# Kernel tuning notes

Hardware: AMD Instinct MI355X
Metric: run time of the kernel (lower is better)

Reference implementation:

```python
import jax, jax.numpy as jnp
import numpy as np

ACT_BIT = 8
W_BIT = 8
EPS = 1e-8


def ste_round(x):
    # straight-through round (matches torch STE quant autograd)
    return x + jax.lax.stop_gradient(jnp.round(x) - x)


def quant_act(x):
    """Per-tensor symmetric 8-bit activation quantization (HAWQ QuantAct)."""
    n = 2 ** (ACT_BIT - 1) - 1  # 127
    x_max = jax.lax.stop_gradient(jnp.max(jnp.abs(x)))
    scale = jnp.maximum(x_max, EPS) / n
    x_int = jnp.clip(ste_round(x / scale), -n - 1, n)
    return x_int * scale, scale


def quant_linear(x_q, act_scale, weight, bias):
    """Per-channel symmetric 8-bit weight quant + integer matmul + fused dequant."""
    n = 2 ** (W_BIT - 1) - 1  # 127
    w_max = jax.lax.stop_gradient(jnp.max(jnp.abs(weight), axis=1, keepdims=True))  # [out,1]
    w_scale = jnp.maximum(w_max, EPS) / n                                            # [out,1]
    w_int = jnp.clip(ste_round(weight / w_scale), -n - 1, n)                         # [out,in]
    bias_scale = w_scale[:, 0] * act_scale                                           # [out]
    b_int = ste_round(bias / bias_scale)                                             # [out]
    x_int = x_q / act_scale                                   # integer-valued float, [..., in]
    out_int = jnp.einsum('...i,oi->...o', x_int, w_int)       # int8-domain GEMM in float
    return (out_int + b_int) * bias_scale                     # fused dequant


def setup_inputs() -> dict:
    key = jax.random.key(0)
    k1, k2, k3 = jax.random.split(key, 3)
    L, B, Q, D, O = 6, 8, 1024, 1024, 1024
    hs = jax.random.normal(k1, (L, B, Q, D), dtype=jnp.float32)
    weight = jax.random.normal(k2, (O, D), dtype=jnp.float32) * 0.02
    bias = jax.random.normal(k3, (O,), dtype=jnp.float32) * 0.02
    return {"hs": hs, "weight": weight, "bias": bias}


def reference(hs, weight, bias):
    x_q, act_scale = quant_act(hs)
    return quant_linear(x_q, act_scale, weight, bias)
```

## Files before the change

kernel.cpp:

```cpp
#include <hip/hip_runtime.h>
#include <stdint.h>

typedef int i32x4 __attribute__((ext_vector_type(4)));

#define K_DIM 1024
#define BM 256
#define BN 256
#define BKK 64
#define NKT (K_DIM / BKK)


__device__ __forceinline__ int quant1(float v, float inv) {
  float t = rintf(v * inv);
  t = fminf(fmaxf(t, -128.0f), 127.0f);
  return (int)t;
}

__device__ __forceinline__ void gld_lds16(const signed char* g, signed char* l) {
  typedef const __attribute__((address_space(1))) unsigned int* gp_t;
  typedef __attribute__((address_space(3))) unsigned int* lp_t;
  __builtin_amdgcn_global_load_lds((gp_t)(const void*)g, (lp_t)(void*)l, 16, 0, 0);
}

#define SB __builtin_amdgcn_sched_barrier(0)
#define BAR __builtin_amdgcn_s_barrier()
#define WAIT_LGKM0 asm volatile("s_waitcnt lgkmcnt(0)" ::: "memory")

__global__ void absmax_part(const float* __restrict__ x, float* __restrict__ parts,
                            long long n4) {
  long long i = (long long)blockIdx.x * blockDim.x + threadIdx.x;
  const long long stride = (long long)gridDim.x * blockDim.x;
  const float4* x4 = (const float4*)x;
  float m = 0.0f;
  for (; i < n4; i += stride) {
    float4 v = x4[i];
    m = fmaxf(m, fmaxf(fmaxf(fabsf(v.x), fabsf(v.y)), fmaxf(fabsf(v.z), fabsf(v.w))));
  }
#pragma unroll
  for (int off = 32; off > 0; off >>= 1) m = fmaxf(m, __shfl_down(m, off, 64));
  __shared__ float sm[4];
  const int lane = threadIdx.x & 63, wid = threadIdx.x >> 6;
  if (lane == 0) sm[wid] = m;
  __syncthreads();
  if (threadIdx.x == 0)
    parts[blockIdx.x] = fmaxf(fmaxf(sm[0], sm[1]), fmaxf(sm[2], sm[3]));
}

__global__ void absmax_fin(const float* __restrict__ parts, unsigned int* __restrict__ amax_u,
                           int nparts) {
  const int t = threadIdx.x;
  float m = 0.0f;
  for (int i = t; i < nparts; i += 256) m = fmaxf(m, parts[i]);
#pragma unroll
  for (int off = 32; off > 0; off >>= 1) m = fmaxf(m, __shfl_down(m, off, 64));
  __shared__ float sm[4];
  const int lane = t & 63, wid = t >> 6;
  if (lane == 0) sm[wid] = m;
  __syncthreads();
  if (t == 0)
    amax_u[0] = __float_as_uint(fmaxf(fmaxf(sm[0], sm[1]), fmaxf(sm[2], sm[3])));
}

__global__ void wquant_kernel(const float* __restrict__ w, const float* __restrict__ bias,
                              const unsigned int* __restrict__ amax_u,
                              signed char* __restrict__ wq,
                              float* __restrict__ bscale, float* __restrict__ bint) {
  const int o = blockIdx.x;
  const int t = threadIdx.x;
  float4 v = ((const float4*)(w + (size_t)o * K_DIM))[t];
  float m = fmaxf(fmaxf(fabsf(v.x), fabsf(v.y)), fmaxf(fabsf(v.z), fabsf(v.w)));
#pragma unroll
  for (int off = 32; off > 0; off >>= 1) m = fmaxf(m, __shfl_down(m, off, 64));
  __shared__ float sm[4];
  __shared__ float s_scale;
  const int lane = t & 63, wid = t >> 6;
  if (lane == 0) sm[wid] = m;
  __syncthreads();
  if (t == 0) {
    float wm = fmaxf(fmaxf(sm[0], sm[1]), fmaxf(sm[2], sm[3]));
    float wsc = fmaxf(wm, 1e-8f) / 127.0f;
    float asc = fmaxf(__uint_as_float(*amax_u), 1e-8f) / 127.0f;
    float bsc = wsc * asc;
    bscale[o] = bsc;
    bint[o] = rintf(bias[o] / bsc);
    s_scale = wsc;
  }
  __syncthreads();
  const float inv = 1.0f / s_scale;
  int q0 = quant1(v.x, inv), q1 = quant1(v.y, inv), q2 = quant1(v.z, inv), q3 = quant1(v.w, inv);
  unsigned int p = (unsigned)(q0 & 255) | ((unsigned)(q1 & 255) << 8) |
                   ((unsigned)(q2 & 255) << 16) | ((unsigned)(q3 & 255) << 24);
  const int F = o >> 4, T = t >> 4;
  const int l = (((t >> 2) & 3) << 4) | (o & 15);
  const int j = (t << 2) & 15;
  *(unsigned int*)(wq + (((size_t)F << 14) + (T << 10) + (l << 4) + j)) = p;
}

__global__ void aquant_kernel(const float* __restrict__ x, const unsigned int* __restrict__ amax_u,
                              uint4* __restrict__ q16, int nchunk) {
  const float asc = fmaxf(__uint_as_float(*amax_u), 1e-8f) / 127.0f;
  const float inv = 1.0f / asc;
  int c = blockIdx.x * blockDim.x + threadIdx.x;
  const int stride = gridDim.x * blockDim.x;
  for (; c < nchunk; c += stride) {
    const int l = c & 63, T = (c >> 6) & 15, F = c >> 10;
    const size_t src = (((size_t)(F << 4) + (l & 15)) << 10) + (T << 6) + ((l >> 4) << 4);
    const float4* s4 = (const float4*)(x + src);
    unsigned int r[4];
#pragma unroll
    for (int q = 0; q < 4; q++) {
      float4 v = s4[q];
      int q0 = quant1(v.x, inv), q1 = quant1(v.y, inv), q2 = quant1(v.z, inv), q3 = quant1(v.w, inv);
      r[q] = (unsigned)(q0 & 255) | ((unsigned)(q1 & 255) << 8) |
             ((unsigned)(q2 & 255) << 16) | ((unsigned)(q3 & 255) << 24);
    }
    q16[c] = make_uint4(r[0], r[1], r[2], r[3]);
  }
}

__global__ __launch_bounds__(512, 2) void gemm_kernel(
    const signed char* __restrict__ A, const signed char* __restrict__ W,
    const float* __restrict__ bscale, const float* __restrict__ bint,
    float* __restrict__ out, int M, int N, int K) {
  extern __shared__ __align__(16) signed char smem[];
  signed char* Abase = smem;

  const int nwg = gridDim.x;
  const int orig = blockIdx.x;
  const int wgid = (orig & 7) * (nwg >> 3) + (orig >> 3);
  const int nbn = N / BN;
  const int bm = wgid / nbn;
  const int bn = wgid % nbn;
  const int m0 = bm * BM, n0 = bn * BN;

  const int tid = threadIdx.x;
  const int lane = tid & 63;
  const int wid = tid >> 6;
  const int wr = wid >> 1 >> 1;
  const int wc = wid & 3;

  const signed char* gaf = A + (((size_t)(m0 >> 4) + wid) << 14) + (lane << 4);
  const size_t fs8 = (size_t)8 << 14;
  const signed char* gbf = W + (((size_t)(n0 >> 4) + wc * 4) << 14) + (lane << 4);

  i32x4 acc[8][4];
#pragma unroll
  for (int i = 0; i < 8; i++)
#pragma unroll
    for (int j = 0; j < 4; j++) acc[i][j] = (i32x4){0, 0, 0, 0};

  i32x4 af[8];
  i32x4 bfA[4], bfB[4];

#define LOADB(L, tt)                                                           \
  do {                                                                         \
    L[0] = *(const i32x4*)(gbf + ((size_t)0 << 14) + ((tt) << 10));            \
    L[1] = *(const i32x4*)(gbf + ((size_t)1 << 14) + ((tt) << 10));            \
    L[2] = *(const i32x4*)(gbf + ((size_t)2 << 14) + ((tt) << 10));            \
    L[3] = *(const i32x4*)(gbf + ((size_t)3 << 14) + ((tt) << 10));            \
  } while (0)

#define ISSUEA(tt)                                                             \
  do {                                                                         \
    gld_lds16(gaf + ((size_t)(tt) << 10),                                      \
              Abase + ((((tt) & 3) * 16 + wid) << 10));                        \
    gld_lds16(gaf + fs8 + ((size_t)(tt) << 10),                                \
              Abase + ((((tt) & 3) * 16 + wid + 8) << 10));                    \
  } while (0)

#define RD_A(t, i_)                                                            \
  af[i_] = *(const i32x4*)(Abase + ((((t) & 3) * 16 + wr * 8 + (i_)) << 10) + (lane << 4))

#define MFMA16U(IB, U)                                                         \
  do {                                                                         \
    __builtin_amdgcn_s_setprio(1);                                             \
    _Pragma("unroll") for (int i_ = 0; i_ < 4; i_++)                           \
      _Pragma("unroll") for (int j_ = 0; j_ < 4; j_++)                         \
        acc[(IB) + i_][j_] = __builtin_amdgcn_mfma_i32_16x16x64_i8(            \
            af[(IB) + i_], U[j_], acc[(IB) + i_][j_], 0, 0, 0);                \
    __builtin_amdgcn_s_setprio(0);                                             \
  } while (0)

#define TILE(t, U, L, DOB, DOA, VMW, DOVM)                                     \
  do {                                                                         \
    if (DOB) LOADB(L, (t) + 1);                                                \
    if (DOA) ISSUEA((t) + 3);                                                  \
    SB;                                                                        \
    RD_A(t, 0); RD_A(t, 1); RD_A(t, 2); RD_A(t, 3);                            \
    RD_A(t, 4); RD_A(t, 5); RD_A(t, 6); RD_A(t, 7);                            \
    MFMA16U(0, U);                                                             \
    MFMA16U(4, U);                                                             \
    if (DOVM) { asm volatile("s_waitcnt " VMW ::: "memory"); }                 \
    SB; BAR; SB;                                                               \
  } while (0)

  ISSUEA(0); ISSUEA(1); ISSUEA(2);
  LOADB(bfA, 0);
  asm volatile("s_waitcnt vmcnt(0)" ::: "memory");
  SB; BAR; SB;

  TILE(0,  bfA, bfB, 1, 1, "vmcnt(8)", 1);
  TILE(1,  bfB, bfA, 1, 1, "vmcnt(8)", 1);
  TILE(2,  bfA, bfB, 1, 1, "vmcnt(8)", 1);
  TILE(3,  bfB, bfA, 1, 1, "vmcnt(8)", 1);
  TILE(4,  bfA, bfB, 1, 1, "vmcnt(8)", 1);
  TILE(5,  bfB, bfA, 1, 1, "vmcnt(8)", 1);
  TILE(6,  bfA, bfB, 1, 1, "vmcnt(8)", 1);
  TILE(7,  bfB, bfA, 1, 1, "vmcnt(8)", 1);
  TILE(8,  bfA, bfB, 1, 1, "vmcnt(8)", 1);
  TILE(9,  bfB, bfA, 1, 1, "vmcnt(8)", 1);
  TILE(10, bfA, bfB, 1, 1, "vmcnt(8)", 1);
  TILE(11, bfB, bfA, 1, 1, "vmcnt(8)", 1);
  TILE(12, bfA, bfB, 1, 1, "vmcnt(8)", 1);
  TILE(13, bfB, bfA, 1, 0, "vmcnt(6)", 1);
  TILE(14, bfA, bfB, 1, 0, "vmcnt(4)", 1);
  TILE(15, bfB, bfA, 0, 0, "", 0);

#undef TILE
#undef MFMA16U
#undef RD_A
#undef ISSUEA
#undef LOADB

  float* Cst = (float*)smem;
  const int rr = (lane >> 4) * 4;
  const int cc = lane & 15;
#pragma unroll
  for (int q = 0; q < 4; ++q) {
    if (wr == (q >> 1)) {
#pragma unroll
      for (int j = 0; j < 4; j++) {
        const int colL = wc * 64 + j * 16 + cc;
        const float bs = bscale[n0 + colL];
        const float bi = bint[n0 + colL];
#pragma unroll
        for (int i2 = 0; i2 < 4; i2++) {
          const int i = (q & 1) * 4 + i2;
#pragma unroll
          for (int r = 0; r < 4; r++)
            Cst[(i2 * 16 + rr + r) * 256 + colL] = ((float)acc[i][j][r] + bi) * bs;
        }
      }
    }
    WAIT_LGKM0;
    BAR;
    const size_t rowbase = (size_t)(m0 + q * 64) * N + n0;
#pragma unroll
    for (int it = 0; it < 8; ++it) {
      const int r_ = it * 8 + wid;
      float4 v = *(const float4*)&Cst[r_ * 256 + lane * 4];
      *(float4*)&out[rowbase + (size_t)r_ * N + lane * 4] = v;
    }
    WAIT_LGKM0;
    BAR;
  }
}

extern "C" void kernel_launch(void* const* d_in, const int* in_sizes, int n_in,
                              void* d_out, int out_size, void* d_ws, size_t ws_size,
                              hipStream_t stream) {
  const float* hs = (const float*)d_in[0];
  const float* w = (const float*)d_in[1];
  const float* bias = (const float*)d_in[2];
  float* out = (float*)d_out;

  const long long n = (long long)in_sizes[0];
  const int K = K_DIM;
  const int O = in_sizes[2];
  const int M = (int)(n / K);

  char* ws = (char*)d_ws;
  unsigned int* amax_u = (unsigned int*)ws;
  float* parts = (float*)(ws + 1024);
  float* bscale = (float*)(ws + 16384);
  float* bint = (float*)(ws + 20480);
  signed char* wq = (signed char*)(ws + 65536);
  signed char* xq = (signed char*)(ws + 65536 + 1048576);

  hipFuncSetAttribute((const void*)gemm_kernel,
                      hipFuncAttributeMaxDynamicSharedMemorySize, 65536);

  const long long n4 = n / 4;
  absmax_part<<<2048, 256, 0, stream>>>(hs, parts, n4);
  absmax_fin<<<1, 256, 0, stream>>>(parts, amax_u, 2048);
  wquant_kernel<<<O, 256, 0, stream>>>(w, bias, amax_u, wq, bscale, bint);
  const int nchunk = (int)(n / 16);
  aquant_kernel<<<2048, 256, 0, stream>>>(hs, amax_u, (uint4*)xq, nchunk);

  const int nblocks = (M / BM) * (O / BN);
  gemm_kernel<<<nblocks, 512, 65536, stream>>>(xq, wq, bscale, bint, out, M, O, K);
}
```

Measured before the change: 180.2 us.

## Double-buffer A fragments in registers to overlap LDS reads with MFMA

```diff
diff --git a/kernel.cpp b/kernel.cpp
--- a/kernel.cpp
+++ b/kernel.cpp
@@ -6,8 +6,7 @@
 #define K_DIM 1024
 #define BM 256
 #define BN 256
-#define BKK 64
-#define NKT (K_DIM / BKK)
+#define NKT 16
 
 
 __device__ __forceinline__ int quant1(float v, float inv) {
@@ -136,7 +135,7 @@
   const int tid = threadIdx.x;
   const int lane = tid & 63;
   const int wid = tid >> 6;
-  const int wr = wid >> 1 >> 1;
+  const int wr = wid >> 2;
   const int wc = wid & 3;
 
   const signed char* gaf = A + (((size_t)(m0 >> 4) + wid) << 14) + (lane << 4);
@@ -149,7 +148,7 @@
 #pragma unroll
     for (int j = 0; j < 4; j++) acc[i][j] = (i32x4){0, 0, 0, 0};
 
-  i32x4 af[8];
+  i32x4 afA[8], afB[8];
   i32x4 bfA[4], bfB[4];
 
 #define LOADB(L, tt)                                                           \
@@ -168,57 +167,61 @@
               Abase + ((((tt) & 3) * 16 + wid + 8) << 10));                    \
   } while (0)
 
-#define RD_A(t, i_)                                                            \
-  af[i_] = *(const i32x4*)(Abase + ((((t) & 3) * 16 + wr * 8 + (i_)) << 10) + (lane << 4))
-
-#define MFMA16U(IB, U)                                                         \
+#define RD_A8(t, AF)                                                           \
+  do {                                                                         \
+    _Pragma("unroll") for (int i_ = 0; i_ < 8; i_++)                           \
+      AF[i_] = *(const i32x4*)(Abase + ((((t) & 3) * 16 + wr * 8 + i_) << 10)  \
+                               + (lane << 4));                                 \
+  } while (0)
+
+#define MFMA32(AF, U)                                                          \
   do {                                                                         \
     __builtin_amdgcn_s_setprio(1);                                             \
-    _Pragma("unroll") for (int i_ = 0; i_ < 4; i_++)                           \
+    _Pragma("unroll") for (int i_ = 0; i_ < 8; i_++)                           \
       _Pragma("unroll") for (int j_ = 0; j_ < 4; j_++)                         \
-        acc[(IB) + i_][j_] = __builtin_amdgcn_mfma_i32_16x16x64_i8(            \
-            af[(IB) + i_], U[j_], acc[(IB) + i_][j_], 0, 0, 0);                \
+        acc[i_][j_] = __builtin_amdgcn_mfma_i32_16x16x64_i8(                   \
+            AF[i_], U[j_], acc[i_][j_], 0, 0, 0);                              \
     __builtin_amdgcn_s_setprio(0);                                             \
   } while (0)
 
-#define TILE(t, U, L, DOB, DOA, VMW, DOVM)                                     \
-  do {                                                                         \
-    if (DOB) LOADB(L, (t) + 1);                                                \
+#define BODY(t, CA, NA, CB, NB, DORD, DOA, DOB, VMW)                           \
+  do {                                                                         \
+    asm volatile("s_waitcnt " VMW ::: "memory");                               \
+    SB; BAR; SB;                                                               \
+    if (DORD) RD_A8((t) + 1, NA);                                              \
     if (DOA) ISSUEA((t) + 3);                                                  \
-    SB;                                                                        \
-    RD_A(t, 0); RD_A(t, 1); RD_A(t, 2); RD_A(t, 3);                            \
-    RD_A(t, 4); RD_A(t, 5); RD_A(t, 6); RD_A(t, 7);                            \
-    MFMA16U(0, U);                                                             \
-    MFMA16U(4, U);                                                             \
-    if (DOVM) { asm volatile("s_waitcnt " VMW ::: "memory"); }                 \
-    SB; BAR; SB;                                                               \
+    if (DOB) LOADB(NB, (t) + 1);                                               \
+    MFMA32(CA, CB);                                                            \
   } while (0)
 
   ISSUEA(0); ISSUEA(1); ISSUEA(2);
   LOADB(bfA, 0);
-  asm volatile("s_waitcnt vmcnt(0)" ::: "memory");
+  asm volatile("s_waitcnt vmcnt(8)" ::: "memory");
   SB; BAR; SB;
-
-  TILE(0,  bfA, bfB, 1, 1, "vmcnt(8)", 1);
-  TILE(1,  bfB, bfA, 1, 1, "vmcnt(8)", 1);
-  TILE(2,  bfA, bfB, 1, 1, "vmcnt(8)", 1);
-  TILE(3,  bfB, bfA, 1, 1, "vmcnt(8)", 1);
-  TILE(4,  bfA, bfB, 1, 1, "vmcnt(8)", 1);
-  TILE(5,  bfB, bfA, 1, 1, "vmcnt(8)", 1);
-  TILE(6,  bfA, bfB, 1, 1, "vmcnt(8)", 1);
-  TILE(7,  bfB, bfA, 1, 1, "vmcnt(8)", 1);
-  TILE(8,  bfA, bfB, 1, 1, "vmcnt(8)", 1);
-  TILE(9,  bfB, bfA, 1, 1, "vmcnt(8)", 1);
-  TILE(10, bfA, bfB, 1, 1, "vmcnt(8)", 1);
-  TILE(11, bfB, bfA, 1, 1, "vmcnt(8)", 1);
-  TILE(12, bfA, bfB, 1, 1, "vmcnt(8)", 1);
-  TILE(13, bfB, bfA, 1, 0, "vmcnt(6)", 1);
-  TILE(14, bfA, bfB, 1, 0, "vmcnt(4)", 1);
-  TILE(15, bfB, bfA, 0, 0, "", 0);
-
-#undef TILE
-#undef MFMA16U
-#undef RD_A
+  RD_A8(0, afA);
+
+  BODY(0,  afA, afB, bfA, bfB, 1, 1, 1, "vmcnt(6)");
+  BODY(1,  afB, afA, bfB, bfA, 1, 1, 1, "vmcnt(6)");
+  BODY(2,  afA, afB, bfA, bfB, 1, 1, 1, "vmcnt(6)");
+  BODY(3,  afB, afA, bfB, bfA, 1, 1, 1, "vmcnt(6)");
+  BODY(4,  afA, afB, bfA, bfB, 1, 1, 1, "vmcnt(6)");
+  BODY(5,  afB, afA, bfB, bfA, 1, 1, 1, "vmcnt(6)");
+  BODY(6,  afA, afB, bfA, bfB, 1, 1, 1, "vmcnt(6)");
+  BODY(7,  afB, afA, bfB, bfA, 1, 1, 1, "vmcnt(6)");
+  BODY(8,  afA, afB, bfA, bfB, 1, 1, 1, "vmcnt(6)");
+  BODY(9,  afB, afA, bfB, bfA, 1, 1, 1, "vmcnt(6)");
+  BODY(10, afA, afB, bfA, bfB, 1, 1, 1, "vmcnt(6)");
+  BODY(11, afB, afA, bfB, bfA, 1, 1, 1, "vmcnt(6)");
+  BODY(12, afA, afB, bfA, bfB, 1, 1, 1, "vmcnt(6)");
+  BODY(13, afB, afA, bfB, bfA, 1, 0, 1, "vmcnt(6)");
+  BODY(14, afA, afB, bfA, bfB, 1, 0, 1, "vmcnt(4)");
+  BODY(15, afB, afA, bfB, bfA, 0, 0, 0, "vmcnt(4)");
+
+  SB; BAR; SB;
+
+#undef BODY
+#undef MFMA32
+#undef RD_A8
 #undef ISSUEA
 #undef LOADB
 
```

Measured after the change: 179.5 us. No clear change (-0.4%).
